# Kernel tuning notes

Measured on AMD Instinct MI355X. Metric: run time of the kernel, lower is better.

Reference implementation:

```python
import jax, jax.numpy as jnp
import numpy as np

B, T, D, F, E, TOP_K = 4, 1024, 1024, 4096, 8, 2


def setup_inputs() -> dict:
    key = jax.random.key(0)
    k0, k1, k2, k3, k4 = jax.random.split(key, 5)
    x = jax.random.normal(k0, (B, T, D), dtype=jnp.float32)
    # xavier-uniform-ish scales
    Wr = jax.random.normal(k1, (D, E), dtype=jnp.float32) * (1.0 / np.sqrt(D))
    W1 = jax.random.normal(k2, (E, D, F), dtype=jnp.float32) * (1.0 / np.sqrt(D))
    W3 = jax.random.normal(k3, (E, D, F), dtype=jnp.float32) * (1.0 / np.sqrt(D))
    W2 = jax.random.normal(k4, (E, F, D), dtype=jnp.float32) * (1.0 / np.sqrt(F))
    return {"x": x, "Wr": Wr, "W1": W1, "W3": W3, "W2": W2}


def reference(x, Wr, W1, W3, W2):
    # Router: logits [B,T,E]
    logits = jnp.einsum('btd,de->bte', x, Wr)
    top_vals, top_idx = jax.lax.top_k(logits, TOP_K)          # [B,T,K]
    weights = jax.nn.softmax(top_vals, axis=-1)               # [B,T,K]
    probs = jax.nn.softmax(logits, axis=-1)                   # [B,T,E]
    usage = probs.mean(axis=(0, 1))                           # [E]
    load_balancing_loss = E * jnp.sum(usage ** 2)

    # SwiGLU experts computed densely per expert: down(silu(gate(x)) * up(x))
    gate = jnp.einsum('btd,edf->ebtf', x, W1)                 # [E,B,T,F]
    up = jnp.einsum('btd,edf->ebtf', x, W3)
    h = jax.nn.silu(gate) * up
    eout = jnp.einsum('ebtf,efd->ebtd', h, W2)                # [E,B,T,D]
    eout = jnp.moveaxis(eout, 0, 2)                           # [B,T,E,D]

    # Gather selected experts and combine with softmax weights
    sel = jnp.take_along_axis(eout, top_idx[..., None], axis=2)  # [B,T,K,D]
    output = jnp.sum(sel * weights[..., None], axis=2)           # [B,T,D]
    return output, load_balancing_loss
```

## Files before the change

### kernel.cpp

```cpp
#include <hip/hip_runtime.h>
#include <hip/hip_bf16.h>
#include <stdint.h>
#include <math.h>

#define NTOK 4096
#define DDIM 1024
#define FDIM 4096
#define NEXP 8
#define NPAIR 8192

#define RT_TPW 8
#define RT_BLOCKS (NTOK / (4 * RT_TPW))

using short8 = __attribute__((ext_vector_type(8))) short;
using f32x4  = __attribute__((ext_vector_type(4))) float;

__device__ __forceinline__ uint16_t f2bf(float f) {
    union { float f; uint32_t u; } v; v.f = f;
    uint32_t r = v.u + 0x7FFFu + ((v.u >> 16) & 1u);
    return (uint16_t)(r >> 16);
}

__device__ __forceinline__ void async16(const void* g, void* l) {
    __builtin_amdgcn_global_load_lds((const __attribute__((address_space(1))) void*)g,
                                     (__attribute__((address_space(3))) void*)l,
                                     16, 0, 0);
}

__global__ void router_kernel(const float* __restrict__ x, const float* __restrict__ Wr,
                              int* __restrict__ cnt_part, float* __restrict__ us_part,
                              int* __restrict__ top_e, float* __restrict__ top_w) {
    __shared__ float us[NEXP];
    __shared__ int cs[NEXP];
    const int tid = threadIdx.x;
    const int wv = tid >> 6;
    const int lane = tid & 63;
    if (tid < NEXP) { us[tid] = 0.f; cs[tid] = 0; }
    __syncthreads();

    for (int i = 0; i < RT_TPW; i++) {
        const int t = blockIdx.x * (4 * RT_TPW) + wv * RT_TPW + i;
        float acc[NEXP];
#pragma unroll
        for (int e = 0; e < NEXP; e++) acc[e] = 0.f;
        const float* xr = x + (size_t)t * DDIM;
        for (int d = lane; d < DDIM; d += 64) {
            float xv = xr[d];
            const float* wr = Wr + (size_t)d * NEXP;
#pragma unroll
            for (int e = 0; e < NEXP; e++) acc[e] += xv * wr[e];
        }
#pragma unroll
        for (int e = 0; e < NEXP; e++) {
#pragma unroll
            for (int off = 32; off > 0; off >>= 1) acc[e] += __shfl_xor(acc[e], off, 64);
        }
        if (lane == 0) {
            int i0 = 0;
#pragma unroll
            for (int e = 1; e < NEXP; e++) if (acc[e] > acc[i0]) i0 = e;
            int i1 = -1;
#pragma unroll
            for (int e = 0; e < NEXP; e++) {
                if (e == i0) continue;
                if (i1 < 0 || acc[e] > acc[i1]) i1 = e;
            }
            float v0 = acc[i0], v1 = acc[i1];
            float e1 = __expf(v1 - v0);
            float inv = 1.f / (1.f + e1);
            top_e[t * 2 + 0] = i0; top_e[t * 2 + 1] = i1;
            top_w[t * 2 + 0] = inv; top_w[t * 2 + 1] = e1 * inv;
            atomicAdd(&cs[i0], 1);
            atomicAdd(&cs[i1], 1);
            float m = acc[0];
#pragma unroll
            for (int e = 1; e < NEXP; e++) m = fmaxf(m, acc[e]);
            float p[NEXP]; float s = 0.f;
#pragma unroll
            for (int e = 0; e < NEXP; e++) { p[e] = __expf(acc[e] - m); s += p[e]; }
            float is = 1.f / s;
#pragma unroll
            for (int e = 0; e < NEXP; e++) atomicAdd(&us[e], p[e] * is);
        }
    }
    __syncthreads();
    if (tid < NEXP) {
        cnt_part[blockIdx.x * NEXP + tid] = cs[tid];
        us_part[blockIdx.x * NEXP + tid] = us[tid];
    }
}

__global__ void finalize_kernel(const int* __restrict__ cnt_part, const float* __restrict__ us_part,
                                int* __restrict__ counts, int* __restrict__ offs,
                                float* __restrict__ out) {
    __shared__ int c[NEXP];
    __shared__ float u[NEXP];
    const int tid = threadIdx.x;
    if (tid < NEXP) {
        int csum = 0; float usum = 0.f;
        for (int b = 0; b < RT_BLOCKS; b++) {
            csum += cnt_part[b * NEXP + tid];
            usum += us_part[b * NEXP + tid];
        }
        counts[tid] = csum; c[tid] = csum; u[tid] = usum;
    }
    __syncthreads();
    if (tid == 0) {
        int s = 0; float l = 0.f;
#pragma unroll
        for (int e = 0; e < NEXP; e++) {
            offs[e] = s; s += c[e];
            float uu = u[e] * (1.f / (float)NTOK);
            l += uu * uu;
        }
        out[(size_t)NTOK * DDIM] = (float)NEXP * l;
    }
}

__global__ void xcast_kernel(const float* __restrict__ x, uint16_t* __restrict__ xb) {
    int i = blockIdx.x * 256 + threadIdx.x;
    float4 v = ((const float4*)x)[i];
    ushort4 o;
    o.x = f2bf(v.x); o.y = f2bf(v.y); o.z = f2bf(v.z); o.w = f2bf(v.w);
    ((ushort4*)xb)[i] = o;
}

__global__ void transpose_cast_kernel(const float* __restrict__ in, uint16_t* __restrict__ outp,
                                      int R, int C, int sel) {
    __shared__ uint16_t tile[64 * 64];
    const int e = blockIdx.z;
    const float* src = in + (size_t)e * R * C;
    const size_t osz = (size_t)R * C * (sel < 0 ? 1 : 2);
    uint16_t* dst = outp + (size_t)e * osz;
    const int r0 = blockIdx.y * 64, c0 = blockIdx.x * 64;
    const int t = threadIdx.x;
    {
        const int rb = t >> 4;
        const int c4 = t & 15;
#pragma unroll
        for (int i = 0; i < 4; i++) {
            const int r = rb + i * 16;
            float4 v = *(const float4*)(src + (size_t)(r0 + r) * C + c0 + c4 * 4);
            const int rc = (r >> 3);
            const int re = (r & 7);
#pragma unroll
            for (int j = 0; j < 4; j++) {
                const int c = c4 * 4 + j;
                float fv = (j == 0) ? v.x : (j == 1) ? v.y : (j == 2) ? v.z : v.w;
                tile[c * 64 + ((rc ^ (c & 7)) << 3) + re] = f2bf(fv);
            }
        }
    }
    __syncthreads();
    {
        const int cr = t >> 3;
        const int ch = t & 7;
#pragma unroll
        for (int i = 0; i < 2; i++) {
            const int c = cr + i * 32;
            uint4 v = *(const uint4*)&tile[c * 64 + ((ch ^ (c & 7)) << 3)];
            const int oc = c0 + c;
            const int orow = (sel < 0) ? oc : (((oc >> 4) << 5) + sel + (oc & 15));
            *(uint4*)(dst + (size_t)orow * R + r0 + ch * 8) = v;
        }
    }
}

__global__ void scatter_kernel(const int* __restrict__ top_e, const float* __restrict__ top_w,
                               const int* __restrict__ offs, int* __restrict__ fill,
                               int* __restrict__ pair_tok, float* __restrict__ pair_w) {
    __shared__ int lcnt[NEXP];
    __shared__ int lbase[NEXP];
    const int tid = threadIdx.x;
    const int t = blockIdx.x * 256 + tid;
    if (tid < NEXP) lcnt[tid] = 0;
    __syncthreads();
    int e0 = top_e[t * 2 + 0], e1 = top_e[t * 2 + 1];
    int r0 = atomicAdd(&lcnt[e0], 1);
    int r1 = atomicAdd(&lcnt[e1], 1);
    __syncthreads();
    if (tid < NEXP) lbase[tid] = atomicAdd(&fill[tid], lcnt[tid]);
    __syncthreads();
    int p0 = offs[e0] + lbase[e0] + r0;
    int p1 = offs[e1] + lbase[e1] + r1;
    pair_tok[p0] = t; pair_w[p0] = top_w[t * 2 + 0];
    pair_tok[p1] = t; pair_w[p1] = top_w[t * 2 + 1];
}

__global__ __launch_bounds__(512, 2)
void expert_up_kernel(const uint16_t* __restrict__ x_bf,
                      const uint16_t* __restrict__ W13t,
                      const int* __restrict__ counts, const int* __restrict__ offs,
                      const int* __restrict__ pair_tok, uint16_t* __restrict__ h) {
    const int e = blockIdx.z, mt = blockIdx.y, bx = blockIdx.x;
    const int cntAll = counts[e];
    if (mt * 512 >= cntAll) return;
    const int cnt = min(512, cntAll - mt * 512);
    const int pairBase = offs[e] + mt * 512;

    __shared__ uint16_t smem[3 * 20480];

    const int tid = threadIdx.x;
    const int w = tid >> 6, lane = tid & 63;
    const int wr = w >> 1, wc = w & 1;
    const int lr = lane & 15, q = lane >> 4;
    const int aoff = (wr * 128 + lr) * 32 + q * 8;
    const int boff = 16384 + (wc * 64 + lr) * 32 + q * 8;
    const int ldst = tid * 8;
    const int rowid = tid >> 2, chunk = tid & 3;

    const uint16_t* asrc[4];
#pragma unroll
    for (int i = 0; i < 4; i++) {
        int tok = pair_tok[pairBase + min(i * 128 + rowid, cnt - 1)];
        asrc[i] = x_bf + (size_t)tok * DDIM + chunk * 8;
    }
    const uint16_t* bsrc = W13t + (size_t)e * 2 * FDIM * DDIM
                         + (size_t)(bx * 128 + rowid) * DDIM + chunk * 8;

#define UST(kt_, sb_) do { \
    async16(asrc[0] + (kt_) * 32, &smem[(sb_) + ldst]); \
    async16(asrc[1] + (kt_) * 32, &smem[(sb_) + 4096 + ldst]); \
    async16(asrc[2] + (kt_) * 32, &smem[(sb_) + 8192 + ldst]); \
    async16(asrc[3] + (kt_) * 32, &smem[(sb_) + 12288 + ldst]); \
    async16(bsrc + (kt_) * 32, &smem[(sb_) + 16384 + ldst]); } while (0)

    f32x4 acc[8][4];
#pragma unroll
    for (int i = 0; i < 8; i++)
#pragma unroll
        for (int j = 0; j < 4; j++) acc[i][j] = (f32x4){0.f, 0.f, 0.f, 0.f};

    UST(0, 0); UST(1, 20480);
    asm volatile("s_waitcnt vmcnt(5)" ::: "memory");
    __builtin_amdgcn_s_barrier();

    int cur = 0;
    for (int kt = 0; kt < 32; ++kt) {
        const uint16_t* A = &smem[cur];
        short8 bf[4], af[4];
#pragma unroll
        for (int ni = 0; ni < 4; ni++) bf[ni] = *(const short8*)(A + boff + ni * 512);
#pragma unroll
        for (int mi = 0; mi < 4; mi++) af[mi] = *(const short8*)(A + aoff + mi * 512);
        if (kt + 2 < 32) {
            int stg = cur + 2 * 20480; if (stg >= 3 * 20480) stg -= 3 * 20480;
            UST(kt + 2, stg);
        }
        __builtin_amdgcn_s_barrier();
        __builtin_amdgcn_s_setprio(1);
#pragma unroll
        for (int ni = 0; ni < 4; ni++)
#pragma unroll
            for (int mi = 0; mi < 4; mi++)
                acc[mi][ni] = __builtin_amdgcn_mfma_f32_16x16x32_bf16(af[mi], bf[ni], acc[mi][ni], 0, 0, 0);
        __builtin_amdgcn_s_setprio(0);
#pragma unroll
        for (int mi = 0; mi < 4; mi++) af[mi] = *(const short8*)(A + aoff + (mi + 4) * 512);
        __builtin_amdgcn_s_setprio(1);
#pragma unroll
        for (int ni = 0; ni < 4; ni++)
#pragma unroll
            for (int mi = 0; mi < 4; mi++)
                acc[mi + 4][ni] = __builtin_amdgcn_mfma_f32_16x16x32_bf16(af[mi], bf[ni], acc[mi + 4][ni], 0, 0, 0);
        __builtin_amdgcn_s_setprio(0);
        if (kt + 2 < 32)      asm volatile("s_waitcnt vmcnt(5)" ::: "memory");
        else if (kt + 1 < 32) asm volatile("s_waitcnt vmcnt(0)" ::: "memory");
        __builtin_amdgcn_s_barrier();
        cur += 20480; if (cur == 3 * 20480) cur = 0;
    }
#undef UST

#pragma unroll
    for (int mi = 0; mi < 8; mi++) {
#pragma unroll
        for (int r = 0; r < 4; r++) {
            const int rowLocal = wr * 128 + mi * 16 + q * 4 + r;
            if (rowLocal < cnt) {
                uint16_t* dst = h + (size_t)(pairBase + rowLocal) * FDIM + bx * 64 + lr;
#pragma unroll
                for (int j = 0; j < 2; j++) {
                    float g = acc[mi][2 * j][r];
                    float u = acc[mi][2 * j + 1][r];
                    float hv = (g / (1.f + __expf(-g))) * u;
                    dst[(wc * 2 + j) * 16] = f2bf(hv);
                }
            }
        }
    }
}

__global__ __launch_bounds__(256, 2)
void expert_down_kernel(const uint16_t* __restrict__ h, const uint16_t* __restrict__ W2t,
                        const int* __restrict__ counts, const int* __restrict__ offs,
                        const int* __restrict__ pair_tok, const float* __restrict__ pair_w,
                        float* __restrict__ out) {
    const int e = blockIdx.z, mt = blockIdx.y;
    const int n0 = blockIdx.x * 128;
    const int cntAll = counts[e];
    if (mt * 256 >= cntAll) return;
    const int cnt = min(256, cntAll - mt * 256);
    const int pairBase = offs[e] + mt * 256;

    __shared__ uint16_t smem[3 * 12288];

    const int tid = threadIdx.x;
    const int w = tid >> 6, lane = tid & 63;
    const int wr = w >> 1, wc = w & 1;
    const int lr = lane & 15, q = lane >> 4;
    const int aoff = (wr * 128 + lr) * 32 + q * 8;
    const int boff = 8192 + (wc * 64 + lr) * 32 + q * 8;
    const int ldst = tid * 8;
    const int rowid = tid >> 2, chunk = tid & 3;

    const uint16_t* asrc[4];
#pragma unroll
    for (int i = 0; i < 4; i++) {
        int pr = pairBase + min(i * 64 + rowid, cnt - 1);
        asrc[i] = h + (size_t)pr * FDIM + chunk * 8;
    }
    const uint16_t* w2p = W2t + (size_t)e * FDIM * DDIM;
    const uint16_t* bsrc0 = w2p + (size_t)(n0 + rowid) * FDIM + chunk * 8;
    const uint16_t* bsrc1 = w2p + (size_t)(n0 + 64 + rowid) * FDIM + chunk * 8;

#define DST_(kt_, sb_) do { \
    async16(asrc[0] + (kt_) * 32, &smem[(sb_) + ldst]); \
    async16(asrc[1] + (kt_) * 32, &smem[(sb_) + 2048 + ldst]); \
    async16(asrc[2] + (kt_) * 32, &smem[(sb_) + 4096 + ldst]); \
    async16(asrc[3] + (kt_) * 32, &smem[(sb_) + 6144 + ldst]); \
    async16(bsrc0 + (kt_) * 32, &smem[(sb_) + 8192 + ldst]); \
    async16(bsrc1 + (kt_) * 32, &smem[(sb_) + 10240 + ldst]); } while (0)

    f32x4 acc[8][4];
#pragma unroll
    for (int i = 0; i < 8; i++)
#pragma unroll
        for (int j = 0; j < 4; j++) acc[i][j] = (f32x4){0.f, 0.f, 0.f, 0.f};

    DST_(0, 0); DST_(1, 12288);
    asm volatile("s_waitcnt vmcnt(6)" ::: "memory");
    __builtin_amdgcn_s_barrier();

    int cur = 0;
    for (int kt = 0; kt < 128; ++kt) {
        const uint16_t* A = &smem[cur];
        short8 bf[4], af[4];
#pragma unroll
        for (int ni = 0; ni < 4; ni++) bf[ni] = *(const short8*)(A + boff + ni * 512);
#pragma unroll
        for (int mi = 0; mi < 4; mi++) af[mi] = *(const short8*)(A + aoff + mi * 512);
        if (kt + 2 < 128) {
            int stg = cur + 2 * 12288; if (stg >= 3 * 12288) stg -= 3 * 12288;
            DST_(kt + 2, stg);
        }
        __builtin_amdgcn_s_barrier();
        __builtin_amdgcn_s_setprio(1);
#pragma unroll
        for (int ni = 0; ni < 4; ni++)
#pragma unroll
            for (int mi = 0; mi < 4; mi++)
                acc[mi][ni] = __builtin_amdgcn_mfma_f32_16x16x32_bf16(af[mi], bf[ni], acc[mi][ni], 0, 0, 0);
        __builtin_amdgcn_s_setprio(0);
#pragma unroll
        for (int mi = 0; mi < 4; mi++) af[mi] = *(const short8*)(A + aoff + (mi + 4) * 512);
        __builtin_amdgcn_s_setprio(1);
#pragma unroll
        for (int ni = 0; ni < 4; ni++)
#pragma unroll
            for (int mi = 0; mi < 4; mi++)
                acc[mi + 4][ni] = __builtin_amdgcn_mfma_f32_16x16x32_bf16(af[mi], bf[ni], acc[mi + 4][ni], 0, 0, 0);
        __builtin_amdgcn_s_setprio(0);
        if (kt + 2 < 128)      asm volatile("s_waitcnt vmcnt(6)" ::: "memory");
        else if (kt + 1 < 128) asm volatile("s_waitcnt vmcnt(0)" ::: "memory");
        __builtin_amdgcn_s_barrier();
        cur += 12288; if (cur == 3 * 12288) cur = 0;
    }
#undef DST_

#pragma unroll
    for (int mi = 0; mi < 8; mi++) {
#pragma unroll
        for (int r = 0; r < 4; r++) {
            const int rowLocal = wr * 128 + mi * 16 + q * 4 + r;
            if (rowLocal < cnt) {
                int pi = pairBase + rowLocal;
                int tok = pair_tok[pi];
                float wgt = pair_w[pi];
                float* dst = out + (size_t)tok * DDIM + n0 + wc * 64 + lr;
#pragma unroll
                for (int ni = 0; ni < 4; ni++)
                    atomicAdd(&dst[ni * 16], acc[mi][ni][r] * wgt);
            }
        }
    }
}

extern "C" void kernel_launch(void* const* d_in, const int* in_sizes, int n_in,
                              void* d_out, int out_size, void* d_ws, size_t ws_size,
                              hipStream_t stream) {
    (void)in_sizes; (void)n_in; (void)ws_size;
    const float* x  = (const float*)d_in[0];
    const float* Wr = (const float*)d_in[1];
    const float* W1 = (const float*)d_in[2];
    const float* W3 = (const float*)d_in[3];
    const float* W2 = (const float*)d_in[4];
    float* out = (float*)d_out;

    char* ws = (char*)d_ws;
    size_t off = 0;
    int*      counts    = (int*)(ws + off);  off += 64;
    int*      offs      = (int*)(ws + off);  off += 64;
    int*      fill      = (int*)(ws + off);  off += 128;
    int*      top_e     = (int*)(ws + off);  off += 4 * NPAIR;
    float*    top_w     = (float*)(ws + off); off += 4 * NPAIR;
    int*      pair_tok  = (int*)(ws + off);  off += 4 * NPAIR;
    float*    pair_w    = (float*)(ws + off); off += 4 * NPAIR;
    int*      cnt_part  = (int*)(ws + off);  off += 4 * RT_BLOCKS * NEXP;
    float*    us_part   = (float*)(ws + off); off += 4 * RT_BLOCKS * NEXP;
    uint16_t* x_bf      = (uint16_t*)(ws + off); off += (size_t)2 * NTOK * DDIM;
    uint16_t* h         = (uint16_t*)(ws + off); off += (size_t)2 * NPAIR * FDIM;
    const size_t wBytes = (size_t)2 * NEXP * DDIM * FDIM;
    uint16_t* W13t = (uint16_t*)(ws + off);
    uint16_t* W2t  = (uint16_t*)(ws + off + 2 * wBytes);

    hipMemsetAsync(ws, 0, 256, stream);
    hipMemsetAsync(d_out, 0, (size_t)out_size * sizeof(float), stream);

    xcast_kernel<<<NTOK * DDIM / 1024, 256, 0, stream>>>(x, x_bf);
    router_kernel<<<RT_BLOCKS, 256, 0, stream>>>(x, Wr, cnt_part, us_part, top_e, top_w);
    finalize_kernel<<<1, 64, 0, stream>>>(cnt_part, us_part, counts, offs, out);
    scatter_kernel<<<NTOK / 256, 256, 0, stream>>>(top_e, top_w, offs, fill, pair_tok, pair_w);

    transpose_cast_kernel<<<dim3(FDIM / 64, DDIM / 64, NEXP), 256, 0, stream>>>(W1, W13t, DDIM, FDIM, 0);
    transpose_cast_kernel<<<dim3(FDIM / 64, DDIM / 64, NEXP), 256, 0, stream>>>(W3, W13t, DDIM, FDIM, 16);
    transpose_cast_kernel<<<dim3(DDIM / 64, FDIM / 64, NEXP), 256, 0, stream>>>(W2, W2t, FDIM, DDIM, -1);

    dim3 gA(2 * FDIM / 128, NTOK / 512, NEXP);
    expert_up_kernel<<<gA, 512, 0, stream>>>(x_bf, W13t, counts, offs, pair_tok, h);
    dim3 gB(DDIM / 128, NTOK / 256, NEXP);
    expert_down_kernel<<<gB, 256, 0, stream>>>(h, W2t, counts, offs, pair_tok, pair_w, out);
}
```

Measured before the change: 842.6 us.

## Reshape up-GEMM tile, add XOR-swizzled LDS layout and inline-asm ds_read scheduling

The up-projection kernel's block tile changes from 512 pairs by 128 columns to 256 pairs by 256 columns, with eight waves arranged 2x4 and fewer async loads per thread. Both expert GEMM kernels now store and read their LDS tiles with an XOR swizzle to avoid bank conflicts. All fragments are issued as inline-asm ds_read_b128 instructions at the start of each step, with partial lgkmcnt waits so the first half of the MFMAs can begin before every read has landed. The hand-written waits and sched barriers take away some of the compiler's scheduling freedom, and the new tile shape changes grid size and per-block reuse.

```diff
diff --git a/kernel.cpp b/kernel.cpp
--- a/kernel.cpp
+++ b/kernel.cpp
@@ -26,6 +26,9 @@
                                      (__attribute__((address_space(3))) void*)l,
                                      16, 0, 0);
 }
+
+#define DSREAD(dst_, addr_, IMM_) \
+    asm volatile("ds_read_b128 %0, %1 offset:" #IMM_ : "=v"(dst_) : "v"(addr_))
 
 __global__ void router_kernel(const float* __restrict__ x, const float* __restrict__ Wr,
                               int* __restrict__ cnt_part, float* __restrict__ us_part,
@@ -194,36 +197,38 @@
                       const int* __restrict__ pair_tok, uint16_t* __restrict__ h) {
     const int e = blockIdx.z, mt = blockIdx.y, bx = blockIdx.x;
     const int cntAll = counts[e];
-    if (mt * 512 >= cntAll) return;
-    const int cnt = min(512, cntAll - mt * 512);
-    const int pairBase = offs[e] + mt * 512;
-
-    __shared__ uint16_t smem[3 * 20480];
+    if (mt * 256 >= cntAll) return;
+    const int cnt = min(256, cntAll - mt * 256);
+    const int pairBase = offs[e] + mt * 256;
+
+    __shared__ uint16_t smem[3 * 16384];
 
     const int tid = threadIdx.x;
     const int w = tid >> 6, lane = tid & 63;
-    const int wr = w >> 1, wc = w & 1;
+    const int wr = w >> 2, wc = w & 3;
     const int lr = lane & 15, q = lane >> 4;
-    const int aoff = (wr * 128 + lr) * 32 + q * 8;
-    const int boff = 16384 + (wc * 64 + lr) * 32 + q * 8;
-    const int ldst = tid * 8;
-    const int rowid = tid >> 2, chunk = tid & 3;
-
-    const uint16_t* asrc[4];
-#pragma unroll
-    for (int i = 0; i < 4; i++) {
-        int tok = pair_tok[pairBase + min(i * 128 + rowid, cnt - 1)];
-        asrc[i] = x_bf + (size_t)tok * DDIM + chunk * 8;
-    }
-    const uint16_t* bsrc = W13t + (size_t)e * 2 * FDIM * DDIM
-                         + (size_t)(bx * 128 + rowid) * DDIM + chunk * 8;
+    const int qa = q ^ ((lr >> 1) & 3);
+    const uint32_t lds0 = (uint32_t)(uintptr_t)&smem[0];
+    const uint32_t aoffB = (uint32_t)((wr * 128 + lr) * 64 + qa * 16);
+    const uint32_t boffB = (uint32_t)(16384 + (wc * 64 + lr) * 64 + qa * 16);
+
+    const int rowid = tid >> 2;
+    const int q_src = (tid & 3) ^ ((tid >> 3) & 3);
+
+    const int tok0 = pair_tok[pairBase + min(rowid, cnt - 1)];
+    const int tok1 = pair_tok[pairBase + min(128 + rowid, cnt - 1)];
+    const uint16_t* asrc0 = x_bf + (size_t)tok0 * DDIM + q_src * 8;
+    const uint16_t* asrc1 = x_bf + (size_t)tok1 * DDIM + q_src * 8;
+    const uint16_t* bsrc0 = W13t + (size_t)e * 2 * FDIM * DDIM
+                          + (size_t)(bx * 256 + rowid) * DDIM + q_src * 8;
+    const uint16_t* bsrc1 = bsrc0 + (size_t)128 * DDIM;
 
 #define UST(kt_, sb_) do { \
-    async16(asrc[0] + (kt_) * 32, &smem[(sb_) + ldst]); \
-    async16(asrc[1] + (kt_) * 32, &smem[(sb_) + 4096 + ldst]); \
-    async16(asrc[2] + (kt_) * 32, &smem[(sb_) + 8192 + ldst]); \
-    async16(asrc[3] + (kt_) * 32, &smem[(sb_) + 12288 + ldst]); \
-    async16(bsrc + (kt_) * 32, &smem[(sb_) + 16384 + ldst]); } while (0)
+    char* Lb = (char*)smem + (sb_) + tid * 16; \
+    async16(asrc0 + (kt_) * 32, Lb); \
+    async16(asrc1 + (kt_) * 32, Lb + 8192); \
+    async16(bsrc0 + (kt_) * 32, Lb + 16384); \
+    async16(bsrc1 + (kt_) * 32, Lb + 24576); } while (0)
 
     f32x4 acc[8][4];
 #pragma unroll
@@ -231,43 +236,57 @@
 #pragma unroll
         for (int j = 0; j < 4; j++) acc[i][j] = (f32x4){0.f, 0.f, 0.f, 0.f};
 
-    UST(0, 0); UST(1, 20480);
-    asm volatile("s_waitcnt vmcnt(5)" ::: "memory");
+    UST(0, 0); UST(1, 32768);
+    asm volatile("s_waitcnt vmcnt(4)" ::: "memory");
     __builtin_amdgcn_s_barrier();
 
-    int cur = 0;
+    uint32_t rb = 0, wb = 65536;
     for (int kt = 0; kt < 32; ++kt) {
-        const uint16_t* A = &smem[cur];
-        short8 bf[4], af[4];
-#pragma unroll
-        for (int ni = 0; ni < 4; ni++) bf[ni] = *(const short8*)(A + boff + ni * 512);
-#pragma unroll
-        for (int mi = 0; mi < 4; mi++) af[mi] = *(const short8*)(A + aoff + mi * 512);
-        if (kt + 2 < 32) {
-            int stg = cur + 2 * 20480; if (stg >= 3 * 20480) stg -= 3 * 20480;
-            UST(kt + 2, stg);
-        }
+        const uint32_t aaddr = lds0 + rb + aoffB;
+        const uint32_t baddr = lds0 + rb + boffB;
+        short8 af0, af1, af2, af3, af4, af5, af6, af7, bf0, bf1, bf2, bf3;
+        DSREAD(af0, aaddr, 0);
+        DSREAD(af1, aaddr, 1024);
+        DSREAD(af2, aaddr, 2048);
+        DSREAD(af3, aaddr, 3072);
+        DSREAD(bf0, baddr, 0);
+        DSREAD(bf1, baddr, 1024);
+        DSREAD(bf2, baddr, 2048);
+        DSREAD(bf3, baddr, 3072);
+        DSREAD(af4, aaddr, 4096);
+        DSREAD(af5, aaddr, 5120);
+        DSREAD(af6, aaddr, 6144);
+        DSREAD(af7, aaddr, 7168);
+        if (kt < 30) UST(kt + 2, wb);
+        asm volatile("s_waitcnt lgkmcnt(4)" ::: "memory");
+        __builtin_amdgcn_sched_barrier(0);
+        __builtin_amdgcn_s_setprio(1);
+#pragma unroll
+        for (int ni = 0; ni < 4; ni++) {
+            const short8 bb = (ni == 0) ? bf0 : (ni == 1) ? bf1 : (ni == 2) ? bf2 : bf3;
+            acc[0][ni] = __builtin_amdgcn_mfma_f32_16x16x32_bf16(af0, bb, acc[0][ni], 0, 0, 0);
+            acc[1][ni] = __builtin_amdgcn_mfma_f32_16x16x32_bf16(af1, bb, acc[1][ni], 0, 0, 0);
+            acc[2][ni] = __builtin_amdgcn_mfma_f32_16x16x32_bf16(af2, bb, acc[2][ni], 0, 0, 0);
+            acc[3][ni] = __builtin_amdgcn_mfma_f32_16x16x32_bf16(af3, bb, acc[3][ni], 0, 0, 0);
+        }
+        __builtin_amdgcn_s_setprio(0);
+        asm volatile("s_waitcnt lgkmcnt(0)" ::: "memory");
+        __builtin_amdgcn_sched_barrier(0);
+        __builtin_amdgcn_s_setprio(1);
+#pragma unroll
+        for (int ni = 0; ni < 4; ni++) {
+            const short8 bb = (ni == 0) ? bf0 : (ni == 1) ? bf1 : (ni == 2) ? bf2 : bf3;
+            acc[4][ni] = __builtin_amdgcn_mfma_f32_16x16x32_bf16(af4, bb, acc[4][ni], 0, 0, 0);
+            acc[5][ni] = __builtin_amdgcn_mfma_f32_16x16x32_bf16(af5, bb, acc[5][ni], 0, 0, 0);
+            acc[6][ni] = __builtin_amdgcn_mfma_f32_16x16x32_bf16(af6, bb, acc[6][ni], 0, 0, 0);
+            acc[7][ni] = __builtin_amdgcn_mfma_f32_16x16x32_bf16(af7, bb, acc[7][ni], 0, 0, 0);
+        }
+        __builtin_amdgcn_s_setprio(0);
+        if (kt < 30)       asm volatile("s_waitcnt vmcnt(4)" ::: "memory");
+        else if (kt == 30) asm volatile("s_waitcnt vmcnt(0)" ::: "memory");
         __builtin_amdgcn_s_barrier();
-        __builtin_amdgcn_s_setprio(1);
-#pragma unroll
-        for (int ni = 0; ni < 4; ni++)
-#pragma unroll
-            for (int mi = 0; mi < 4; mi++)
-                acc[mi][ni] = __builtin_amdgcn_mfma_f32_16x16x32_bf16(af[mi], bf[ni], acc[mi][ni], 0, 0, 0);
-        __builtin_amdgcn_s_setprio(0);
-#pragma unroll
-        for (int mi = 0; mi < 4; mi++) af[mi] = *(const short8*)(A + aoff + (mi + 4) * 512);
-        __builtin_amdgcn_s_setprio(1);
-#pragma unroll
-        for (int ni = 0; ni < 4; ni++)
-#pragma unroll
-            for (int mi = 0; mi < 4; mi++)
-                acc[mi + 4][ni] = __builtin_amdgcn_mfma_f32_16x16x32_bf16(af[mi], bf[ni], acc[mi + 4][ni], 0, 0, 0);
-        __builtin_amdgcn_s_setprio(0);
-        if (kt + 2 < 32)      asm volatile("s_waitcnt vmcnt(5)" ::: "memory");
-        else if (kt + 1 < 32) asm volatile("s_waitcnt vmcnt(0)" ::: "memory");
-        __builtin_amdgcn_s_barrier();
-        cur += 20480; if (cur == 3 * 20480) cur = 0;
+        rb += 32768; if (rb == 98304) rb = 0;
+        wb += 32768; if (wb == 98304) wb = 0;
     }
 #undef UST
 
@@ -277,7 +296,7 @@
         for (int r = 0; r < 4; r++) {
             const int rowLocal = wr * 128 + mi * 16 + q * 4 + r;
             if (rowLocal < cnt) {
-                uint16_t* dst = h + (size_t)(pairBase + rowLocal) * FDIM + bx * 64 + lr;
+                uint16_t* dst = h + (size_t)(pairBase + rowLocal) * FDIM + bx * 128 + lr;
 #pragma unroll
                 for (int j = 0; j < 2; j++) {
                     float g = acc[mi][2 * j][r];
@@ -308,28 +327,32 @@
     const int w = tid >> 6, lane = tid & 63;
     const int wr = w >> 1, wc = w & 1;
     const int lr = lane & 15, q = lane >> 4;
-    const int aoff = (wr * 128 + lr) * 32 + q * 8;
-    const int boff = 8192 + (wc * 64 + lr) * 32 + q * 8;
-    const int ldst = tid * 8;
-    const int rowid = tid >> 2, chunk = tid & 3;
+    const int qa = q ^ ((lr >> 1) & 3);
+    const uint32_t lds0 = (uint32_t)(uintptr_t)&smem[0];
+    const uint32_t aoffB = (uint32_t)((wr * 128 + lr) * 64 + qa * 16);
+    const uint32_t boffB = (uint32_t)(16384 + (wc * 64 + lr) * 64 + qa * 16);
+
+    const int rowid = tid >> 2;
+    const int q_src = (tid & 3) ^ ((tid >> 3) & 3);
 
     const uint16_t* asrc[4];
 #pragma unroll
     for (int i = 0; i < 4; i++) {
         int pr = pairBase + min(i * 64 + rowid, cnt - 1);
-        asrc[i] = h + (size_t)pr * FDIM + chunk * 8;
+        asrc[i] = h + (size_t)pr * FDIM + q_src * 8;
     }
     const uint16_t* w2p = W2t + (size_t)e * FDIM * DDIM;
-    const uint16_t* bsrc0 = w2p + (size_t)(n0 + rowid) * FDIM + chunk * 8;
-    const uint16_t* bsrc1 = w2p + (size_t)(n0 + 64 + rowid) * FDIM + chunk * 8;
+    const uint16_t* bsrc0 = w2p + (size_t)(n0 + rowid) * FDIM + q_src * 8;
+    const uint16_t* bsrc1 = bsrc0 + (size_t)64 * FDIM;
 
 #define DST_(kt_, sb_) do { \
-    async16(asrc[0] + (kt_) * 32, &smem[(sb_) + ldst]); \
-    async16(asrc[1] + (kt_) * 32, &smem[(sb_) + 2048 + ldst]); \
-    async16(asrc[2] + (kt_) * 32, &smem[(sb_) + 4096 + ldst]); \
-    async16(asrc[3] + (kt_) * 32, &smem[(sb_) + 6144 + ldst]); \
-    async16(bsrc0 + (kt_) * 32, &smem[(sb_) + 8192 + ldst]); \
-    async16(bsrc1 + (kt_) * 32, &smem[(sb_) + 10240 + ldst]); } while (0)
+    char* Lb = (char*)smem + (sb_) + tid * 16; \
+    async16(asrc[0] + (kt_) * 32, Lb); \
+    async16(asrc[1] + (kt_) * 32, Lb + 4096); \
+    async16(asrc[2] + (kt_) * 32, Lb + 8192); \
+    async16(asrc[3] + (kt_) * 32, Lb + 12288); \
+    async16(bsrc0 + (kt_) * 32, Lb + 16384); \
+    async16(bsrc1 + (kt_) * 32, Lb + 20480); } while (0)
 
     f32x4 acc[8][4];
 #pragma unroll
@@ -337,43 +360,57 @@
 #pragma unroll
         for (int j = 0; j < 4; j++) acc[i][j] = (f32x4){0.f, 0.f, 0.f, 0.f};
 
-    DST_(0, 0); DST_(1, 12288);
+    DST_(0, 0); DST_(1, 24576);
     asm volatile("s_waitcnt vmcnt(6)" ::: "memory");
     __builtin_amdgcn_s_barrier();
 
-    int cur = 0;
+    uint32_t rb = 0, wb = 49152;
     for (int kt = 0; kt < 128; ++kt) {
-        const uint16_t* A = &smem[cur];
-        short8 bf[4], af[4];
-#pragma unroll
-        for (int ni = 0; ni < 4; ni++) bf[ni] = *(const short8*)(A + boff + ni * 512);
-#pragma unroll
-        for (int mi = 0; mi < 4; mi++) af[mi] = *(const short8*)(A + aoff + mi * 512);
-        if (kt + 2 < 128) {
-            int stg = cur + 2 * 12288; if (stg >= 3 * 12288) stg -= 3 * 12288;
-            DST_(kt + 2, stg);
-        }
+        const uint32_t aaddr = lds0 + rb + aoffB;
+        const uint32_t baddr = lds0 + rb + boffB;
+        short8 af0, af1, af2, af3, af4, af5, af6, af7, bf0, bf1, bf2, bf3;
+        DSREAD(af0, aaddr, 0);
+        DSREAD(af1, aaddr, 1024);
+        DSREAD(af2, aaddr, 2048);
+        DSREAD(af3, aaddr, 3072);
+        DSREAD(bf0, baddr, 0);
+        DSREAD(bf1, baddr, 1024);
+        DSREAD(bf2, baddr, 2048);
+        DSREAD(bf3, baddr, 3072);
+        DSREAD(af4, aaddr, 4096);
+        DSREAD(af5, aaddr, 5120);
+        DSREAD(af6, aaddr, 6144);
+        DSREAD(af7, aaddr, 7168);
+        if (kt < 126) DST_(kt + 2, wb);
+        asm volatile("s_waitcnt lgkmcnt(4)" ::: "memory");
+        __builtin_amdgcn_sched_barrier(0);
+        __builtin_amdgcn_s_setprio(1);
+#pragma unroll
+        for (int ni = 0; ni < 4; ni++) {
+            const short8 bb = (ni == 0) ? bf0 : (ni == 1) ? bf1 : (ni == 2) ? bf2 : bf3;
+            acc[0][ni] = __builtin_amdgcn_mfma_f32_16x16x32_bf16(af0, bb, acc[0][ni], 0, 0, 0);
+            acc[1][ni] = __builtin_amdgcn_mfma_f32_16x16x32_bf16(af1, bb, acc[1][ni], 0, 0, 0);
+            acc[2][ni] = __builtin_amdgcn_mfma_f32_16x16x32_bf16(af2, bb, acc[2][ni], 0, 0, 0);
+            acc[3][ni] = __builtin_amdgcn_mfma_f32_16x16x32_bf16(af3, bb, acc[3][ni], 0, 0, 0);
+        }
+        __builtin_amdgcn_s_setprio(0);
+        asm volatile("s_waitcnt lgkmcnt(0)" ::: "memory");
+        __builtin_amdgcn_sched_barrier(0);
+        __builtin_amdgcn_s_setprio(1);
+#pragma unroll
+        for (int ni = 0; ni < 4; ni++) {
+            const short8 bb = (ni == 0) ? bf0 : (ni == 1) ? bf1 : (ni == 2) ? bf2 : bf3;
+            acc[4][ni] = __builtin_amdgcn_mfma_f32_16x16x32_bf16(af4, bb, acc[4][ni], 0, 0, 0);
+            acc[5][ni] = __builtin_amdgcn_mfma_f32_16x16x32_bf16(af5, bb, acc[5][ni], 0, 0, 0);
+            acc[6][ni] = __builtin_amdgcn_mfma_f32_16x16x32_bf16(af6, bb, acc[6][ni], 0, 0, 0);
+            acc[7][ni] = __builtin_amdgcn_mfma_f32_16x16x32_bf16(af7, bb, acc[7][ni], 0, 0, 0);
+        }
+        __builtin_amdgcn_s_setprio(0);
+        if (kt < 126)       asm volatile("s_waitcnt vmcnt(6)" ::: "memory");
+        else if (kt == 126) asm volatile("s_waitcnt vmcnt(0)" ::: "memory");
         __builtin_amdgcn_s_barrier();
-        __builtin_amdgcn_s_setprio(1);
-#pragma unroll
-        for (int ni = 0; ni < 4; ni++)
-#pragma unroll
-            for (int mi = 0; mi < 4; mi++)
-                acc[mi][ni] = __builtin_amdgcn_mfma_f32_16x16x32_bf16(af[mi], bf[ni], acc[mi][ni], 0, 0, 0);
-        __builtin_amdgcn_s_setprio(0);
-#pragma unroll
-        for (int mi = 0; mi < 4; mi++) af[mi] = *(const short8*)(A + aoff + (mi + 4) * 512);
-        __builtin_amdgcn_s_setprio(1);
-#pragma unroll
-        for (int ni = 0; ni < 4; ni++)
-#pragma unroll
-            for (int mi = 0; mi < 4; mi++)
-                acc[mi + 4][ni] = __builtin_amdgcn_mfma_f32_16x16x32_bf16(af[mi], bf[ni], acc[mi + 4][ni], 0, 0, 0);
-        __builtin_amdgcn_s_setprio(0);
-        if (kt + 2 < 128)      asm volatile("s_waitcnt vmcnt(6)" ::: "memory");
-        else if (kt + 1 < 128) asm volatile("s_waitcnt vmcnt(0)" ::: "memory");
-        __builtin_amdgcn_s_barrier();
-        cur += 12288; if (cur == 3 * 12288) cur = 0;
+        rb += 24576; if (rb == 73728) rb = 0;
+        wb += 24576; if (wb == 73728) wb = 0;
     }
 #undef DST_
 
@@ -435,7 +472,7 @@
     transpose_cast_kernel<<<dim3(FDIM / 64, DDIM / 64, NEXP), 256, 0, stream>>>(W3, W13t, DDIM, FDIM, 16);
     transpose_cast_kernel<<<dim3(DDIM / 64, FDIM / 64, NEXP), 256, 0, stream>>>(W2, W2t, FDIM, DDIM, -1);
 
-    dim3 gA(2 * FDIM / 128, NTOK / 512, NEXP);
+    dim3 gA(2 * FDIM / 256, NTOK / 256, NEXP);
     expert_up_kernel<<<gA, 512, 0, stream>>>(x_bf, W13t, counts, offs, pair_tok, h);
     dim3 gB(DDIM / 128, NTOK / 256, NEXP);
     expert_down_kernel<<<gB, 256, 0, stream>>>(h, W2t, counts, offs, pair_tok, pair_w, out);
```

Result: faster. 794.5 us (-5.7%).
